# Performance work log

Hardware: AMD Instinct MI355X
Metric: run time of the kernel (lower is better)

The kernel has to match this reference:

```python
import jax, jax.numpy as jnp
import numpy as np

POS_T = 0.7
NEG_T = 0.3


def setup_inputs() -> dict:
    key = jax.random.key(0)
    k1, k2 = jax.random.split(key)
    pred_boxes = jax.random.uniform(k1, (8, 50000, 4), dtype=jnp.float32)
    gt_boxes = jax.random.uniform(k2, (8, 64, 4), dtype=jnp.float32)
    return {"pred_boxes": pred_boxes, "gt_boxes": gt_boxes}


def _cxcywh_to_xyxy(b):
    cx, cy, w, h = jnp.split(b, 4, axis=-1)
    return jnp.concatenate([cx - 0.5 * w, cy - 0.5 * h, cx + 0.5 * w, cy + 0.5 * h], axis=-1)


def _pairwise_iou(gt_xyxy, pr_xyxy):
    # gt_xyxy: [B,G,4], pr_xyxy: [B,N,4] -> ious [B,G,N]
    gt = gt_xyxy[:, :, None, :]   # [B,G,1,4]
    pr = pr_xyxy[:, None, :, :]   # [B,1,N,4]
    lt = jnp.maximum(gt[..., :2], pr[..., :2])
    rb = jnp.minimum(gt[..., 2:], pr[..., 2:])
    wh = jnp.clip(rb - lt, 0.0)
    inter = wh[..., 0] * wh[..., 1]                                   # [B,G,N]
    area_g = (gt[..., 2] - gt[..., 0]) * (gt[..., 3] - gt[..., 1])    # [B,G,1]
    area_p = (pr[..., 2] - pr[..., 0]) * (pr[..., 3] - pr[..., 1])    # [B,1,N]
    return inter / (area_g + area_p - inter)


def reference(pred_boxes, gt_boxes):
    # Dense-mask equivalent of the original ragged index lists:
    #   pos_mask[b,g,n] = True iff pred n is a positive match for gt g
    #                     (iou > POS_T, plus the per-gt argmax pred)
    #   neg_mask[b,n]   = True iff max_g iou < NEG_T
    ious = _pairwise_iou(_cxcywh_to_xyxy(gt_boxes), _cxcywh_to_xyxy(pred_boxes))  # [B,G,N]
    N = ious.shape[-1]
    best = jnp.argmax(ious, axis=-1)                                   # [B,G]
    argmax_onehot = jnp.arange(N)[None, None, :] == best[..., None]    # [B,G,N]
    pos_mask = (ious > POS_T) | argmax_onehot
    neg_mask = jnp.max(ious, axis=1) < NEG_T                           # [B,N]
    return ious, pos_mask, neg_mask
```

## Files before the change

### kernel.cpp

```cpp
#include <hip/hip_runtime.h>
#include <cstdint>
#include <cstddef>

#define NB 8
#define NG 64
#define NP 50000
#define NBLK 98
#define NSTREAM (NBLK * NB)
#define NPCH 32
#define PCH 1563
#define NAMAX (NPCH * (NG / 8) * NB)

__device__ __forceinline__ void opaque(float& x) { asm volatile("" : "+v"(x)); }
__device__ __forceinline__ unsigned long long umax64(unsigned long long a, unsigned long long b) {
    return a > b ? a : b;
}

template<bool WITH_ARGMAX>
__global__ __launch_bounds__(256) void fused_main(
    const float* __restrict__ pred,
    const float* __restrict__ gt,
    float* __restrict__ out_iou,
    float* __restrict__ out_pos,
    float* __restrict__ out_neg,
    unsigned long long* __restrict__ part)
{
    const int bid = blockIdx.x;
    const int tid = threadIdx.x;

    if (!WITH_ARGMAX || bid < NSTREAM) {
        __shared__ float s_gx0[NG], s_gy0[NG], s_gx1[NG], s_gy1[NG], s_ga[NG];
        const int b  = bid / NBLK;
        const int bx = bid % NBLK;

        if (tid < NG) {
            const float4 gb = reinterpret_cast<const float4*>(gt)[b * NG + tid];
            float hw = 0.5f * gb.z, hh = 0.5f * gb.w;
            float x0 = gb.x - hw, y0 = gb.y - hh;
            float x1 = gb.x + hw, y1 = gb.y + hh;
            float ga = (x1 - x0) * (y1 - y0);
            opaque(ga);
            s_gx0[tid] = x0; s_gy0[tid] = y0;
            s_gx1[tid] = x1; s_gy1[tid] = y1;
            s_ga[tid]  = ga;
        }
        __syncthreads();

        const int p = 2 * (bx * 256 + tid);
        if (p >= NP) return;

        const float4 pb0 = reinterpret_cast<const float4*>(pred)[(size_t)b * NP + p];
        const float4 pb1 = reinterpret_cast<const float4*>(pred)[(size_t)b * NP + p + 1];

        float hw0 = 0.5f * pb0.z, hh0 = 0.5f * pb0.w;
        const float ax0 = pb0.x - hw0, ay0 = pb0.y - hh0;
        const float ax1 = pb0.x + hw0, ay1 = pb0.y + hh0;
        float pa0 = (ax1 - ax0) * (ay1 - ay0);
        opaque(pa0);

        float hw1 = 0.5f * pb1.z, hh1 = 0.5f * pb1.w;
        const float bx0 = pb1.x - hw1, by0 = pb1.y - hh1;
        const float bx1 = pb1.x + hw1, by1 = pb1.y + hh1;
        float pa1 = (bx1 - bx0) * (by1 - by0);
        opaque(pa1);

        float maxv0 = 0.0f, maxv1 = 0.0f;
        const size_t base = (size_t)b * NG * NP + (size_t)p;

        #pragma unroll 8
        for (int g = 0; g < NG; ++g) {
            const float gx0 = s_gx0[g], gy0 = s_gy0[g];
            const float gx1 = s_gx1[g], gy1 = s_gy1[g];
            const float ga  = s_ga[g];

            float w0 = fmaxf(fminf(gx1, ax1) - fmaxf(gx0, ax0), 0.0f);
            float h0 = fmaxf(fminf(gy1, ay1) - fmaxf(gy0, ay0), 0.0f);
            float inter0 = w0 * h0;
            opaque(inter0);
            float iou0 = inter0 / ((ga + pa0) - inter0);

            float w1 = fmaxf(fminf(gx1, bx1) - fmaxf(gx0, bx0), 0.0f);
            float h1 = fmaxf(fminf(gy1, by1) - fmaxf(gy0, by0), 0.0f);
            float inter1 = w1 * h1;
            opaque(inter1);
            float iou1 = inter1 / ((ga + pa1) - inter1);

            float2 vi; vi.x = iou0; vi.y = iou1;
            *reinterpret_cast<float2*>(out_iou + base + (size_t)g * NP) = vi;

            float2 vp; vp.x = (iou0 > 0.7f) ? 1.0f : 0.0f;
                       vp.y = (iou1 > 0.7f) ? 1.0f : 0.0f;
            *reinterpret_cast<float2*>(out_pos + base + (size_t)g * NP) = vp;

            maxv0 = fmaxf(maxv0, iou0);
            maxv1 = fmaxf(maxv1, iou1);
        }

        float2 vn; vn.x = (maxv0 < 0.3f) ? 1.0f : 0.0f;
                   vn.y = (maxv1 < 0.3f) ? 1.0f : 0.0f;
        *reinterpret_cast<float2*>(out_neg + (size_t)b * NP + p) = vn;
    } else {
        __shared__ float a_gx0[8], a_gy0[8], a_gx1[8], a_gy1[8], a_ga[8];
        __shared__ unsigned long long s_part[8][4];

        const int a     = bid - NSTREAM;
        const int chunk = a % NPCH;
        const int t2    = a / NPCH;
        const int gg    = t2 % (NG / 8);
        const int b     = t2 / (NG / 8);
        const int p0    = chunk * PCH;

        if (tid < 8) {
            const float4 gb = reinterpret_cast<const float4*>(gt)[b * NG + gg * 8 + tid];
            float hw = 0.5f * gb.z, hh = 0.5f * gb.w;
            float x0 = gb.x - hw, y0 = gb.y - hh;
            float x1 = gb.x + hw, y1 = gb.y + hh;
            float ga = (x1 - x0) * (y1 - y0);
            opaque(ga);
            a_gx0[tid] = x0; a_gy0[tid] = y0;
            a_gx1[tid] = x1; a_gy1[tid] = y1;
            a_ga[tid]  = ga;
        }
        __syncthreads();

        float        bv[8] = {-1.f,-1.f,-1.f,-1.f,-1.f,-1.f,-1.f,-1.f};
        unsigned int bp[8] = {0,0,0,0,0,0,0,0};

        for (int i = tid; i < PCH; i += 256) {
            const int p = p0 + i;
            if (p >= NP) break;
            const float4 pb = reinterpret_cast<const float4*>(pred)[(size_t)b * NP + p];
            float hw = 0.5f * pb.z, hh = 0.5f * pb.w;
            const float px0 = pb.x - hw, py0 = pb.y - hh;
            const float px1 = pb.x + hw, py1 = pb.y + hh;
            float pa = (px1 - px0) * (py1 - py0);
            opaque(pa);

            #pragma unroll
            for (int j = 0; j < 8; ++j) {
                float w = fmaxf(fminf(a_gx1[j], px1) - fmaxf(a_gx0[j], px0), 0.0f);
                float h = fmaxf(fminf(a_gy1[j], py1) - fmaxf(a_gy0[j], py0), 0.0f);
                float inter = w * h;
                opaque(inter);
                float iou = inter / ((a_ga[j] + pa) - inter);
                if (iou > bv[j]) { bv[j] = iou; bp[j] = (unsigned int)p; }
            }
        }

        const int lane = tid & 63;
        const int wv = tid >> 6;
        #pragma unroll
        for (int j = 0; j < 8; ++j) {
            unsigned long long k = 0;
            if (bv[j] >= 0.0f)
                k = ((unsigned long long)__float_as_uint(bv[j]) << 32) |
                    (unsigned long long)(0xFFFFFFFFu - bp[j]);
            #pragma unroll
            for (int s = 1; s < 64; s <<= 1)
                k = umax64(k, __shfl_xor(k, s, 64));
            if (lane == 0) s_part[j][wv] = k;
        }
        __syncthreads();

        if (tid < 8) {
            unsigned long long r = umax64(umax64(s_part[tid][0], s_part[tid][1]),
                                          umax64(s_part[tid][2], s_part[tid][3]));
            part[((size_t)b * NG + (size_t)(gg * 8 + tid)) * NPCH + chunk] = r;
        }
    }
}

__global__ __launch_bounds__(256) void pos_fix(
    const unsigned long long* __restrict__ part,
    float* __restrict__ out_pos)
{
    const int row = blockIdx.x * 256 + threadIdx.x;
    if (row >= NB * NG) return;
    const unsigned long long* pr = part + (size_t)row * NPCH;
    unsigned long long r = pr[0];
    #pragma unroll
    for (int c = 1; c < NPCH; ++c) r = umax64(r, pr[c]);
    unsigned int idx = 0xFFFFFFFFu - (unsigned int)(r & 0xFFFFFFFFull);
    if (idx < NP) out_pos[(size_t)row * NP + idx] = 1.0f;
}

__global__ __launch_bounds__(256) void argmax_scan(
    const float* __restrict__ out_iou,
    float* __restrict__ out_pos)
{
    const int row = blockIdx.x;
    const float4* r4 = reinterpret_cast<const float4*>(out_iou + (size_t)row * NP);

    float bv = -1.0f;
    int   bi = 0x7fffffff;
    for (int c = threadIdx.x; c < NP / 4; c += 256) {
        float4 v = r4[c];
        int p = 4 * c;
        if (v.x > bv) { bv = v.x; bi = p; }
        if (v.y > bv) { bv = v.y; bi = p + 1; }
        if (v.z > bv) { bv = v.z; bi = p + 2; }
        if (v.w > bv) { bv = v.w; bi = p + 3; }
    }
    #pragma unroll
    for (int s = 1; s < 64; s <<= 1) {
        float ov = __shfl_xor(bv, s, 64);
        int   oi = __shfl_xor(bi, s, 64);
        if (ov > bv || (ov == bv && oi < bi)) { bv = ov; bi = oi; }
    }
    __shared__ float sv[4];
    __shared__ int   si[4];
    const int wid = threadIdx.x >> 6;
    if ((threadIdx.x & 63) == 0) { sv[wid] = bv; si[wid] = bi; }
    __syncthreads();
    if (threadIdx.x == 0) {
        for (int w = 1; w < 4; ++w)
            if (sv[w] > bv || (sv[w] == bv && si[w] < bi)) { bv = sv[w]; bi = si[w]; }
        out_pos[(size_t)row * NP + bi] = 1.0f;
    }
}

extern "C" void kernel_launch(void* const* d_in, const int* in_sizes, int n_in,
                              void* d_out, int out_size, void* d_ws, size_t ws_size,
                              hipStream_t stream) {
    const float* pred = (const float*)d_in[0];
    const float* gt   = (const float*)d_in[1];
    float* out_iou = (float*)d_out;
    float* out_pos = out_iou + (size_t)NB * NG * NP;
    float* out_neg = out_pos + (size_t)NB * NG * NP;

    const size_t part_bytes = (size_t)NB * NG * NPCH * sizeof(unsigned long long);

    if (ws_size >= part_bytes) {
        unsigned long long* part = (unsigned long long*)d_ws;
        fused_main<true><<<dim3(NSTREAM + NAMAX), dim3(256), 0, stream>>>(
            pred, gt, out_iou, out_pos, out_neg, part);
        pos_fix<<<dim3((NB * NG + 255) / 256), dim3(256), 0, stream>>>(part, out_pos);
    } else {
        fused_main<false><<<dim3(NSTREAM), dim3(256), 0, stream>>>(
            pred, gt, out_iou, out_pos, out_neg, nullptr);
        argmax_scan<<<dim3(NB * NG), dim3(256), 0, stream>>>(out_iou, out_pos);
    }
}
```

Before: 55.01 us.

## Split GT boxes across two block halves and process four preds per thread

The streaming part of the fused kernel now gives each thread four predicted boxes, using float4 stores, and splits the 64 GT boxes into two halves handled by separate blocks. This creates more, shorter blocks and wider stores. Per-half max IoU values are written to a workspace buffer, and the follow-up kernel now combines them into the negative mask as well as applying the argmax fix. This adds extra workspace traffic, a larger workspace requirement, and more register pressure from four boxes per thread.

```diff
diff --git a/kernel.cpp b/kernel.cpp
--- a/kernel.cpp
+++ b/kernel.cpp
@@ -5,36 +5,43 @@
 #define NB 8
 #define NG 64
 #define NP 50000
-#define NBLK 98
-#define NSTREAM (NBLK * NB)
+#define NQ (NP / 4)
+#define GH 2
+#define GPH (NG / GH)
+#define PBLK 49
+#define NSTREAM (PBLK * GH * NB)
 #define NPCH 32
 #define PCH 1563
 #define NAMAX (NPCH * (NG / 8) * NB)
+#define NTOT (NSTREAM + NAMAX)
+#define NNEGB ((NB * NQ + 255) / 256)
 
 __device__ __forceinline__ void opaque(float& x) { asm volatile("" : "+v"(x)); }
 __device__ __forceinline__ unsigned long long umax64(unsigned long long a, unsigned long long b) {
     return a > b ? a : b;
 }
 
-template<bool WITH_ARGMAX>
+
 __global__ __launch_bounds__(256) void fused_main(
     const float* __restrict__ pred,
     const float* __restrict__ gt,
     float* __restrict__ out_iou,
     float* __restrict__ out_pos,
-    float* __restrict__ out_neg,
+    float* __restrict__ negpart,
     unsigned long long* __restrict__ part)
 {
     const int bid = blockIdx.x;
     const int tid = threadIdx.x;
 
-    if (!WITH_ARGMAX || bid < NSTREAM) {
-        __shared__ float s_gx0[NG], s_gy0[NG], s_gx1[NG], s_gy1[NG], s_ga[NG];
-        const int b  = bid / NBLK;
-        const int bx = bid % NBLK;
-
-        if (tid < NG) {
-            const float4 gb = reinterpret_cast<const float4*>(gt)[b * NG + tid];
+    if (bid < NSTREAM) {
+        __shared__ float s_gx0[GPH], s_gy0[GPH], s_gx1[GPH], s_gy1[GPH], s_ga[GPH];
+        const int b  = bid / (PBLK * GH);
+        const int r  = bid % (PBLK * GH);
+        const int pc = r / GH;
+        const int gh = r % GH;
+
+        if (tid < GPH) {
+            const float4 gb = reinterpret_cast<const float4*>(gt)[b * NG + gh * GPH + tid];
             float hw = 0.5f * gb.z, hh = 0.5f * gb.w;
             float x0 = gb.x - hw, y0 = gb.y - hh;
             float x1 = gb.x + hw, y1 = gb.y + hh;
@@ -46,59 +53,56 @@
         }
         __syncthreads();
 
-        const int p = 2 * (bx * 256 + tid);
-        if (p >= NP) return;
-
-        const float4 pb0 = reinterpret_cast<const float4*>(pred)[(size_t)b * NP + p];
-        const float4 pb1 = reinterpret_cast<const float4*>(pred)[(size_t)b * NP + p + 1];
-
-        float hw0 = 0.5f * pb0.z, hh0 = 0.5f * pb0.w;
-        const float ax0 = pb0.x - hw0, ay0 = pb0.y - hh0;
-        const float ax1 = pb0.x + hw0, ay1 = pb0.y + hh0;
-        float pa0 = (ax1 - ax0) * (ay1 - ay0);
-        opaque(pa0);
-
-        float hw1 = 0.5f * pb1.z, hh1 = 0.5f * pb1.w;
-        const float bx0 = pb1.x - hw1, by0 = pb1.y - hh1;
-        const float bx1 = pb1.x + hw1, by1 = pb1.y + hh1;
-        float pa1 = (bx1 - bx0) * (by1 - by0);
-        opaque(pa1);
-
-        float maxv0 = 0.0f, maxv1 = 0.0f;
+        const int pt = pc * 256 + tid;
+        if (pt >= NQ) return;
+        const int p = 4 * pt;
+
+        float px0[4], py0[4], px1[4], py1[4], pa[4];
+        #pragma unroll
+        for (int k = 0; k < 4; ++k) {
+            const float4 pb = reinterpret_cast<const float4*>(pred)[(size_t)b * NP + p + k];
+            float hw = 0.5f * pb.z, hh = 0.5f * pb.w;
+            px0[k] = pb.x - hw; py0[k] = pb.y - hh;
+            px1[k] = pb.x + hw; py1[k] = pb.y + hh;
+            float a = (px1[k] - px0[k]) * (py1[k] - py0[k]);
+            opaque(a);
+            pa[k] = a;
+        }
+
+        float maxv[4] = {0.0f, 0.0f, 0.0f, 0.0f};
         const size_t base = (size_t)b * NG * NP + (size_t)p;
 
-        #pragma unroll 8
-        for (int g = 0; g < NG; ++g) {
-            const float gx0 = s_gx0[g], gy0 = s_gy0[g];
-            const float gx1 = s_gx1[g], gy1 = s_gy1[g];
-            const float ga  = s_ga[g];
-
-            float w0 = fmaxf(fminf(gx1, ax1) - fmaxf(gx0, ax0), 0.0f);
-            float h0 = fmaxf(fminf(gy1, ay1) - fmaxf(gy0, ay0), 0.0f);
-            float inter0 = w0 * h0;
-            opaque(inter0);
-            float iou0 = inter0 / ((ga + pa0) - inter0);
-
-            float w1 = fmaxf(fminf(gx1, bx1) - fmaxf(gx0, bx0), 0.0f);
-            float h1 = fmaxf(fminf(gy1, by1) - fmaxf(gy0, by0), 0.0f);
-            float inter1 = w1 * h1;
-            opaque(inter1);
-            float iou1 = inter1 / ((ga + pa1) - inter1);
-
-            float2 vi; vi.x = iou0; vi.y = iou1;
-            *reinterpret_cast<float2*>(out_iou + base + (size_t)g * NP) = vi;
-
-            float2 vp; vp.x = (iou0 > 0.7f) ? 1.0f : 0.0f;
-                       vp.y = (iou1 > 0.7f) ? 1.0f : 0.0f;
-            *reinterpret_cast<float2*>(out_pos + base + (size_t)g * NP) = vp;
-
-            maxv0 = fmaxf(maxv0, iou0);
-            maxv1 = fmaxf(maxv1, iou1);
-        }
-
-        float2 vn; vn.x = (maxv0 < 0.3f) ? 1.0f : 0.0f;
-                   vn.y = (maxv1 < 0.3f) ? 1.0f : 0.0f;
-        *reinterpret_cast<float2*>(out_neg + (size_t)b * NP + p) = vn;
+        #pragma unroll 4
+        for (int gi = 0; gi < GPH; ++gi) {
+            const int g = gh * GPH + gi;
+            const float gx0 = s_gx0[gi], gy0 = s_gy0[gi];
+            const float gx1 = s_gx1[gi], gy1 = s_gy1[gi];
+            const float ga  = s_ga[gi];
+
+            float iou[4];
+            #pragma unroll
+            for (int k = 0; k < 4; ++k) {
+                float w = fmaxf(fminf(gx1, px1[k]) - fmaxf(gx0, px0[k]), 0.0f);
+                float h = fmaxf(fminf(gy1, py1[k]) - fmaxf(gy0, py0[k]), 0.0f);
+                float inter = w * h;
+                opaque(inter);
+                iou[k] = inter / ((ga + pa[k]) - inter);
+                maxv[k] = fmaxf(maxv[k], iou[k]);
+            }
+
+            float4 vi; vi.x = iou[0]; vi.y = iou[1]; vi.z = iou[2]; vi.w = iou[3];
+            *reinterpret_cast<float4*>(out_iou + base + (size_t)g * NP) = vi;
+
+            float4 vp;
+            vp.x = (iou[0] > 0.7f) ? 1.0f : 0.0f;
+            vp.y = (iou[1] > 0.7f) ? 1.0f : 0.0f;
+            vp.z = (iou[2] > 0.7f) ? 1.0f : 0.0f;
+            vp.w = (iou[3] > 0.7f) ? 1.0f : 0.0f;
+            *reinterpret_cast<float4*>(out_pos + base + (size_t)g * NP) = vp;
+        }
+
+        float4 mn; mn.x = maxv[0]; mn.y = maxv[1]; mn.z = maxv[2]; mn.w = maxv[3];
+        *reinterpret_cast<float4*>(negpart + ((size_t)b * GH + gh) * NP + p) = mn;
     } else {
         __shared__ float a_gx0[8], a_gy0[8], a_gx1[8], a_gy1[8], a_ga[8];
         __shared__ unsigned long long s_part[8][4];
@@ -170,18 +174,103 @@
     }
 }
 
-__global__ __launch_bounds__(256) void pos_fix(
+__global__ __launch_bounds__(256) void fix_combined(
     const unsigned long long* __restrict__ part,
-    float* __restrict__ out_pos)
+    const float* __restrict__ negpart,
+    float* __restrict__ out_pos,
+    float* __restrict__ out_neg)
 {
-    const int row = blockIdx.x * 256 + threadIdx.x;
-    if (row >= NB * NG) return;
-    const unsigned long long* pr = part + (size_t)row * NPCH;
-    unsigned long long r = pr[0];
-    #pragma unroll
-    for (int c = 1; c < NPCH; ++c) r = umax64(r, pr[c]);
-    unsigned int idx = 0xFFFFFFFFu - (unsigned int)(r & 0xFFFFFFFFull);
-    if (idx < NP) out_pos[(size_t)row * NP + idx] = 1.0f;
+    const int bid = blockIdx.x;
+    const int tid = threadIdx.x;
+
+    if (bid < NNEGB) {
+        const int idx = bid * 256 + tid;
+        if (idx < NB * NQ) {
+            const int b = idx / NQ;
+            const int q = idx % NQ;
+            const int p = 4 * q;
+            const float4 m0 = *reinterpret_cast<const float4*>(negpart + ((size_t)b * GH + 0) * NP + p);
+            const float4 m1 = *reinterpret_cast<const float4*>(negpart + ((size_t)b * GH + 1) * NP + p);
+            float4 vn;
+            vn.x = (fmaxf(m0.x, m1.x) < 0.3f) ? 1.0f : 0.0f;
+            vn.y = (fmaxf(m0.y, m1.y) < 0.3f) ? 1.0f : 0.0f;
+            vn.z = (fmaxf(m0.z, m1.z) < 0.3f) ? 1.0f : 0.0f;
+            vn.w = (fmaxf(m0.w, m1.w) < 0.3f) ? 1.0f : 0.0f;
+            *reinterpret_cast<float4*>(out_neg + (size_t)b * NP + p) = vn;
+        }
+    } else {
+        const int row = (bid - NNEGB) * 256 + tid;
+        if (row < NB * NG) {
+            const unsigned long long* pr = part + (size_t)row * NPCH;
+            unsigned long long r = pr[0];
+            #pragma unroll
+            for (int c = 1; c < NPCH; ++c) r = umax64(r, pr[c]);
+            unsigned int idx = 0xFFFFFFFFu - (unsigned int)(r & 0xFFFFFFFFull);
+            if (idx < NP) out_pos[(size_t)row * NP + idx] = 1.0f;
+        }
+    }
+}
+
+__global__ __launch_bounds__(256) void stream2_full(
+    const float* __restrict__ pred,
+    const float* __restrict__ gt,
+    float* __restrict__ out_iou,
+    float* __restrict__ out_pos,
+    float* __restrict__ out_neg)
+{
+    __shared__ float s_gx0[NG], s_gy0[NG], s_gx1[NG], s_gy1[NG], s_ga[NG];
+    const int b = blockIdx.y;
+    const int tid = threadIdx.x;
+    if (tid < NG) {
+        const float4 gb = reinterpret_cast<const float4*>(gt)[b * NG + tid];
+        float hw = 0.5f * gb.z, hh = 0.5f * gb.w;
+        float x0 = gb.x - hw, y0 = gb.y - hh;
+        float x1 = gb.x + hw, y1 = gb.y + hh;
+        float ga = (x1 - x0) * (y1 - y0);
+        opaque(ga);
+        s_gx0[tid] = x0; s_gy0[tid] = y0;
+        s_gx1[tid] = x1; s_gy1[tid] = y1;
+        s_ga[tid]  = ga;
+    }
+    __syncthreads();
+    const int p = 2 * (blockIdx.x * 256 + tid);
+    if (p >= NP) return;
+    const float4 pb0 = reinterpret_cast<const float4*>(pred)[(size_t)b * NP + p];
+    const float4 pb1 = reinterpret_cast<const float4*>(pred)[(size_t)b * NP + p + 1];
+    float hw0 = 0.5f * pb0.z, hh0 = 0.5f * pb0.w;
+    const float ax0 = pb0.x - hw0, ay0 = pb0.y - hh0;
+    const float ax1 = pb0.x + hw0, ay1 = pb0.y + hh0;
+    float pa0 = (ax1 - ax0) * (ay1 - ay0); opaque(pa0);
+    float hw1 = 0.5f * pb1.z, hh1 = 0.5f * pb1.w;
+    const float bx0 = pb1.x - hw1, by0 = pb1.y - hh1;
+    const float bx1 = pb1.x + hw1, by1 = pb1.y + hh1;
+    float pa1 = (bx1 - bx0) * (by1 - by0); opaque(pa1);
+    float maxv0 = 0.0f, maxv1 = 0.0f;
+    const size_t base = (size_t)b * NG * NP + (size_t)p;
+    #pragma unroll 8
+    for (int g = 0; g < NG; ++g) {
+        const float gx0 = s_gx0[g], gy0 = s_gy0[g];
+        const float gx1 = s_gx1[g], gy1 = s_gy1[g];
+        const float ga  = s_ga[g];
+        float w0 = fmaxf(fminf(gx1, ax1) - fmaxf(gx0, ax0), 0.0f);
+        float h0 = fmaxf(fminf(gy1, ay1) - fmaxf(gy0, ay0), 0.0f);
+        float inter0 = w0 * h0; opaque(inter0);
+        float iou0 = inter0 / ((ga + pa0) - inter0);
+        float w1 = fmaxf(fminf(gx1, bx1) - fmaxf(gx0, bx0), 0.0f);
+        float h1 = fmaxf(fminf(gy1, by1) - fmaxf(gy0, by0), 0.0f);
+        float inter1 = w1 * h1; opaque(inter1);
+        float iou1 = inter1 / ((ga + pa1) - inter1);
+        float2 vi; vi.x = iou0; vi.y = iou1;
+        *reinterpret_cast<float2*>(out_iou + base + (size_t)g * NP) = vi;
+        float2 vp; vp.x = (iou0 > 0.7f) ? 1.0f : 0.0f;
+                   vp.y = (iou1 > 0.7f) ? 1.0f : 0.0f;
+        *reinterpret_cast<float2*>(out_pos + base + (size_t)g * NP) = vp;
+        maxv0 = fmaxf(maxv0, iou0);
+        maxv1 = fmaxf(maxv1, iou1);
+    }
+    float2 vn; vn.x = (maxv0 < 0.3f) ? 1.0f : 0.0f;
+               vn.y = (maxv1 < 0.3f) ? 1.0f : 0.0f;
+    *reinterpret_cast<float2*>(out_neg + (size_t)b * NP + p) = vn;
 }
 
 __global__ __launch_bounds__(256) void argmax_scan(
@@ -190,7 +279,6 @@
 {
     const int row = blockIdx.x;
     const float4* r4 = reinterpret_cast<const float4*>(out_iou + (size_t)row * NP);
-
     float bv = -1.0f;
     int   bi = 0x7fffffff;
     for (int c = threadIdx.x; c < NP / 4; c += 256) {
@@ -229,15 +317,16 @@
     float* out_neg = out_pos + (size_t)NB * NG * NP;
 
     const size_t part_bytes = (size_t)NB * NG * NPCH * sizeof(unsigned long long);
-
-    if (ws_size >= part_bytes) {
+    const size_t neg_bytes  = (size_t)NB * GH * NP * sizeof(float);
+
+    if (ws_size >= part_bytes + neg_bytes) {
         unsigned long long* part = (unsigned long long*)d_ws;
-        fused_main<true><<<dim3(NSTREAM + NAMAX), dim3(256), 0, stream>>>(
-            pred, gt, out_iou, out_pos, out_neg, part);
-        pos_fix<<<dim3((NB * NG + 255) / 256), dim3(256), 0, stream>>>(part, out_pos);
+        float* negpart = (float*)((char*)d_ws + part_bytes);
+        fused_main<<<dim3(NTOT), dim3(256), 0, stream>>>(
+            pred, gt, out_iou, out_pos, negpart, part);
+        fix_combined<<<dim3(NNEGB + 2), dim3(256), 0, stream>>>(part, negpart, out_pos, out_neg);
     } else {
-        fused_main<false><<<dim3(NSTREAM), dim3(256), 0, stream>>>(
-            pred, gt, out_iou, out_pos, out_neg, nullptr);
+        stream2_full<<<dim3(98, NB), dim3(256), 0, stream>>>(pred, gt, out_iou, out_pos, out_neg);
         argmax_scan<<<dim3(NB * NG), dim3(256), 0, stream>>>(out_iou, out_pos);
     }
 }
```

New measurement: 58.67 us. +6.7%, slower.
